# Kernel optimization log

Hardware: AMD Instinct MI355X
Metric: run time of the kernel (lower is better)

The kernel has to match this reference:

```python
import jax, jax.numpy as jnp
import numpy as np

N_NODES = 50000
N_EDGES = 600000
IC, H, OC = 64, 128, 32
EPS = 1e-5


def setup_inputs() -> dict:
    key = jax.random.key(0)
    ks = jax.random.split(key, 8)
    x = jax.random.normal(ks[0], (N_NODES, IC), dtype=jnp.float32)
    ei = jax.random.randint(ks[1], (2, N_EDGES), 0, N_NODES, dtype=jnp.int64)
    proj_w = jax.random.normal(ks[2], (IC, H), dtype=jnp.float32) * 0.05
    proj_b = jnp.zeros((H,), dtype=jnp.float32)
    # conv_w[layer, lin, :, :] with lin order: key, query, value, skip
    conv_w = jax.random.normal(ks[3], (3, 4, H, H), dtype=jnp.float32) * 0.05
    conv_b = jnp.zeros((3, 4, H), dtype=jnp.float32)
    bn_gamma = jnp.ones((3, H), dtype=jnp.float32)
    bn_beta = jnp.zeros((3, H), dtype=jnp.float32)
    head_w = jax.random.normal(ks[4], (H, OC), dtype=jnp.float32) * 0.05
    head_b = jnp.zeros((OC,), dtype=jnp.float32)
    return {"x": x, "ei": ei, "proj_w": proj_w, "proj_b": proj_b,
            "conv_w": conv_w, "conv_b": conv_b, "bn_gamma": bn_gamma,
            "bn_beta": bn_beta, "head_w": head_w, "head_b": head_b}


def _res_gated_conv(x, src, dst, w, b):
    # PyG ResGatedGraphConv: out_i = skip(x_i) + sum_j sigmoid(key(x_i)+query(x_j)) * value(x_j)
    k = x @ w[0] + b[0]      # key   (applied to target/dst)
    q = x @ w[1] + b[1]      # query (applied to source/src)
    v = x @ w[2] + b[2]      # value (applied to source/src)
    msg = jax.nn.sigmoid(k[dst] + q[src]) * v[src]          # [E, H]
    agg = jax.ops.segment_sum(msg, dst, num_segments=x.shape[0])  # [N, H]
    return x @ w[3] + b[3] + agg


def _batchnorm(x, gamma, beta):
    # training-mode BatchNorm1d: batch statistics over the node dimension
    mean = jnp.mean(x, axis=0)
    var = jnp.var(x, axis=0)
    return gamma * (x - mean) * jax.lax.rsqrt(var + EPS) + beta


def reference(x, ei, proj_w, proj_b, conv_w, conv_b, bn_gamma, bn_beta, head_w, head_b):
    src, dst = ei[0], ei[1]
    h = jax.nn.relu(x @ proj_w + proj_b)
    for layer in range(3):
        h = _res_gated_conv(h, src, dst, conv_w[layer], conv_b[layer])
        h = jax.nn.relu(_batchnorm(h, bn_gamma[layer], bn_beta[layer]))
        # dropout(p=0.2) is identity in eval mode
    return h @ head_w + head_b
```

## Files before the change

### kernel.cpp

```cpp
#include <hip/hip_runtime.h>
#include <hip/hip_bf16.h>
#include <math.h>

#define HDIM 128
#define ICDIM 64
#define OCDIM 32
#define BN_EPS 1e-5f
#define NCH 64

typedef __attribute__((ext_vector_type(8))) short bv8;
typedef __attribute__((ext_vector_type(4))) float fv4;

static __device__ __forceinline__ unsigned short f2bf(float v) {
    __hip_bfloat16 t = __float2bfloat16(v);
    return *(unsigned short*)&t;
}
static __device__ __forceinline__ float bflo(unsigned int u) {
    union { unsigned int i; float f; } c; c.i = u << 16; return c.f;
}
static __device__ __forceinline__ float bfhi(unsigned int u) {
    union { unsigned int i; float f; } c; c.i = u & 0xffff0000u; return c.f;
}
static __device__ __forceinline__ unsigned int pack2bf(float a, float b) {
    return (unsigned int)f2bf(a) | ((unsigned int)f2bf(b) << 16);
}

__global__ void wprep_kernel(const float* __restrict__ conv_w,
                             const float* __restrict__ proj_w,
                             __hip_bfloat16* __restrict__ Wt,
                             __hip_bfloat16* __restrict__ Wp) {
    int mat = blockIdx.x;
    if (mat < 12) {
        const float* s = conv_w + (size_t)mat * HDIM * HDIM;
        __hip_bfloat16* d = Wt + (size_t)mat * HDIM * HDIM;
        for (int idx = threadIdx.x; idx < HDIM * HDIM; idx += 256) {
            int i = idx >> 7, o = idx & 127;
            d[(size_t)o * HDIM + i] = __float2bfloat16(s[idx]);
        }
    } else {
        for (int idx = threadIdx.x; idx < ICDIM * HDIM; idx += 256) {
            int i = idx >> 7, o = idx & 127;
            Wp[(size_t)o * ICDIM + i] = __float2bfloat16(proj_w[idx]);
        }
    }
}

__global__ __launch_bounds__(256)
void proj_mfma_kernel(const float* __restrict__ x,
                      const __hip_bfloat16* __restrict__ wp,
                      const float* __restrict__ b,
                      __hip_bfloat16* __restrict__ h, int n) {
    __shared__ unsigned int xs[NCH * ICDIM / 2];
    int tid = threadIdx.x;
    int m0 = blockIdx.x * NCH;

    const float2* xsrc = (const float2*)(x + (size_t)m0 * ICDIM);
    for (int i = tid; i < NCH * ICDIM / 2; i += 256) {
        int node = m0 + (i >> 5);
        float2 v = (node < n) ? xsrc[i] : (float2){0.f, 0.f};
        xs[i ^ (((i >> 5) & 7) << 2)] = pack2bf(v.x, v.y);
    }

    int wv = tid >> 6;
    int lane = tid & 63;
    int j = lane & 15;
    int kg = lane >> 4;
    int sw = (j & 7) << 4;

    bv8 af[2][2];
#pragma unroll
    for (int gs = 0; gs < 2; ++gs)
#pragma unroll
        for (int ks = 0; ks < 2; ++ks)
            af[gs][ks] = *(const bv8*)((const unsigned short*)wp +
                (size_t)(wv * 32 + gs * 16 + j) * ICDIM + ks * 32 + kg * 8);

    float4 bias0 = *(const float4*)(b + wv * 32 + kg * 4);
    float4 bias1 = *(const float4*)(b + wv * 32 + 16 + kg * 4);

    __syncthreads();

#pragma unroll
    for (int t4 = 0; t4 < NCH / 16; ++t4) {
        const char* rowbase = (const char*)xs + (t4 * 16 + j) * (ICDIM * 2);
        fv4 acc0 = (fv4){0.f, 0.f, 0.f, 0.f};
        fv4 acc1 = (fv4){0.f, 0.f, 0.f, 0.f};
#pragma unroll
        for (int ks = 0; ks < 2; ++ks) {
            bv8 bf = *(const bv8*)(rowbase + ((kg * 16 + ks * 64) ^ sw));
            acc0 = __builtin_amdgcn_mfma_f32_16x16x32_bf16(af[0][ks], bf, acc0, 0, 0, 0);
            acc1 = __builtin_amdgcn_mfma_f32_16x16x32_bf16(af[1][ks], bf, acc1, 0, 0, 0);
        }
        int node = m0 + t4 * 16 + j;
        if (node < n) {
            unsigned short* o =
                (unsigned short*)h + (size_t)node * HDIM + wv * 32 + kg * 4;
            ushort4 r0, r1;
            r0.x = f2bf(fmaxf(acc0.x + bias0.x, 0.f));
            r0.y = f2bf(fmaxf(acc0.y + bias0.y, 0.f));
            r0.z = f2bf(fmaxf(acc0.z + bias0.z, 0.f));
            r0.w = f2bf(fmaxf(acc0.w + bias0.w, 0.f));
            r1.x = f2bf(fmaxf(acc1.x + bias1.x, 0.f));
            r1.y = f2bf(fmaxf(acc1.y + bias1.y, 0.f));
            r1.z = f2bf(fmaxf(acc1.z + bias1.z, 0.f));
            r1.w = f2bf(fmaxf(acc1.w + bias1.w, 0.f));
            *(ushort4*)o = r0;
            *(ushort4*)(o + 16) = r1;
        }
    }
}

__global__ __launch_bounds__(1024)
void gemm4_fused_kernel(const __hip_bfloat16* __restrict__ hB,
                        const float* __restrict__ Ssrc,
                        const float* __restrict__ stp,
                        const float* __restrict__ gma,
                        const float* __restrict__ bta,
                        const __hip_bfloat16* __restrict__ wt4,
                        const float* __restrict__ b4,
                        __hip_bfloat16* __restrict__ K,
                        unsigned int* __restrict__ QV,
                        float* __restrict__ S, int n) {
    __shared__ unsigned short hs[NCH * HDIM];
    int tid = threadIdx.x;
    int m0 = blockIdx.x * NCH;
    int wsw = ((tid >> 4) & 7) << 4;

    if (Ssrc) {
        const float4* src = (const float4*)(Ssrc + (size_t)m0 * HDIM);
        float4 v0 = src[tid * 2];
        float4 v1 = src[tid * 2 + 1];
        int c0 = (tid * 8) & 127;
        float invn = 1.f / (float)n;
        float vv[8] = {v0.x, v0.y, v0.z, v0.w, v1.x, v1.y, v1.z, v1.w};
        unsigned int* dst = (unsigned int*)((char*)hs + ((tid * 16) ^ wsw));
#pragma unroll
        for (int p = 0; p < 8; p += 2) {
            int c = c0 + p;
            float mA = stp[c] * invn, mB = stp[c + 1] * invn;
            float scA = gma[c] * rsqrtf(stp[128 + c] * invn - mA * mA + BN_EPS);
            float scB = gma[c + 1] * rsqrtf(stp[129 + c] * invn - mB * mB + BN_EPS);
            float shA = bta[c] - mA * scA, shB = bta[c + 1] - mB * scB;
            float rA = fmaxf(fmaf(vv[p], scA, shA), 0.f);
            float rB = fmaxf(fmaf(vv[p + 1], scB, shB), 0.f);
            dst[p >> 1] = pack2bf(rA, rB);
        }
    } else {
        const uint4* src = (const uint4*)((const unsigned short*)hB + (size_t)m0 * HDIM);
        *(uint4*)((char*)hs + ((tid * 16) ^ wsw)) = src[tid];
    }

    int wv = tid >> 6;
    int lane = tid & 63;
    int lin = wv >> 2;
    int g2 = wv & 3;
    int j = lane & 15;
    int kg = lane >> 4;
    int sw = (j & 7) << 4;

    const unsigned short* wbase =
        (const unsigned short*)(wt4 + (size_t)lin * HDIM * HDIM);
    bv8 af[2][4];
#pragma unroll
    for (int gs = 0; gs < 2; ++gs)
#pragma unroll
        for (int ks = 0; ks < 4; ++ks)
            af[gs][ks] = *(const bv8*)(wbase +
                (size_t)(g2 * 32 + gs * 16 + j) * HDIM + ks * 32 + kg * 8);

    const float* bl = b4 + lin * HDIM;
    float4 bias0 = *(const float4*)(bl + g2 * 32 + kg * 4);
    float4 bias1 = *(const float4*)(bl + g2 * 32 + 16 + kg * 4);

    __syncthreads();

#pragma unroll
    for (int t4 = 0; t4 < NCH / 16; ++t4) {
        const char* rowbase = (const char*)hs + (t4 * 16 + j) * (HDIM * 2);
        fv4 acc0 = (fv4){0.f, 0.f, 0.f, 0.f};
        fv4 acc1 = (fv4){0.f, 0.f, 0.f, 0.f};
#pragma unroll
        for (int ks = 0; ks < 4; ++ks) {
            bv8 bf = *(const bv8*)(rowbase + ((kg * 16 + ks * 64) ^ sw));
            acc0 = __builtin_amdgcn_mfma_f32_16x16x32_bf16(af[0][ks], bf, acc0, 0, 0, 0);
            acc1 = __builtin_amdgcn_mfma_f32_16x16x32_bf16(af[1][ks], bf, acc1, 0, 0, 0);
        }
        int node = m0 + t4 * 16 + j;
        if (node >= n) continue;
        int c0 = g2 * 32 + kg * 4;
        float f0 = acc0.x + bias0.x, f1 = acc0.y + bias0.y;
        float f2 = acc0.z + bias0.z, f3 = acc0.w + bias0.w;
        float f4 = acc1.x + bias1.x, f5 = acc1.y + bias1.y;
        float f6 = acc1.z + bias1.z, f7 = acc1.w + bias1.w;
        if (lin == 3) {
            float* o = S + (size_t)node * HDIM + c0;
            *(float4*)o = (float4){f0, f1, f2, f3};
            *(float4*)(o + 16) = (float4){f4, f5, f6, f7};
        } else if (lin == 0) {
            unsigned short* o = (unsigned short*)K + (size_t)node * HDIM + c0;
            *(ushort4*)o = (ushort4){f2bf(f0), f2bf(f1), f2bf(f2), f2bf(f3)};
            *(ushort4*)(o + 16) = (ushort4){f2bf(f4), f2bf(f5), f2bf(f6), f2bf(f7)};
        } else {
            unsigned int* o = QV + (size_t)node * HDIM + c0 + (lin - 1);
            o[0] = pack2bf(f0, f1);
            o[2] = pack2bf(f2, f3);
            o[16] = pack2bf(f4, f5);
            o[18] = pack2bf(f6, f7);
        }
    }
}

__global__ void hist_kernel(const int* __restrict__ ei, int* __restrict__ deg, int e) {
    int i = blockIdx.x * 256 + threadIdx.x;
    if (i < e) atomicAdd(&deg[ei[(size_t)e + i]], 1);
}

__global__ void scan1_kernel(const int* __restrict__ deg, int* __restrict__ incl,
                             int* __restrict__ bsum, int n) {
    __shared__ int tmp[256];
    int i = blockIdx.x * 256 + threadIdx.x;
    int v = (i < n) ? deg[i] : 0;
    tmp[threadIdx.x] = v;
    __syncthreads();
    for (int ofs = 1; ofs < 256; ofs <<= 1) {
        int t = (threadIdx.x >= ofs) ? tmp[threadIdx.x - ofs] : 0;
        __syncthreads();
        tmp[threadIdx.x] += t;
        __syncthreads();
    }
    if (i < n) incl[i] = tmp[threadIdx.x];
    if (threadIdx.x == 255) bsum[blockIdx.x] = tmp[255];
}

__global__ void scan2_kernel(int* __restrict__ bsum, int nb) {
    __shared__ int tmp[256];
    int v = (threadIdx.x < nb) ? bsum[threadIdx.x] : 0;
    tmp[threadIdx.x] = v;
    __syncthreads();
    for (int ofs = 1; ofs < 256; ofs <<= 1) {
        int t = (threadIdx.x >= ofs) ? tmp[threadIdx.x - ofs] : 0;
        __syncthreads();
        tmp[threadIdx.x] += t;
        __syncthreads();
    }
    if (threadIdx.x < nb) bsum[threadIdx.x] = tmp[threadIdx.x] - v;
}

__global__ void scan3_kernel(const int* __restrict__ deg, const int* __restrict__ incl,
                             const int* __restrict__ bsum, int* __restrict__ off,
                             int* __restrict__ cursor, int n, int e) {
    int i = blockIdx.x * 256 + threadIdx.x;
    if (i < n) {
        int ex = incl[i] - deg[i] + bsum[blockIdx.x];
        off[i] = ex;
        cursor[i] = ex;
        if (i == n - 1) off[n] = e;
    }
}

__global__ void scatter_kernel(const int* __restrict__ ei, int* __restrict__ cursor,
                               int* __restrict__ esrc, int e) {
    int i = blockIdx.x * 256 + threadIdx.x;
    if (i < e) {
        int dst = ei[(size_t)e + i];
        int pos = atomicAdd(&cursor[dst], 1);
        esrc[pos] = ei[i];
    }
}

__global__ void agg_kernel(const int* __restrict__ off, const int* __restrict__ esrc,
                           const __hip_bfloat16* __restrict__ kb,
                           const unsigned int* __restrict__ QV,
                           float* __restrict__ S, int n) {
    int d = blockIdx.x * 4 + (threadIdx.x >> 6);
    if (d >= n) return;
    int lane = threadIdx.x & 63;
    const uint2* qvw = (const uint2*)QV;
    unsigned int kwu = ((const unsigned int*)kb)[(size_t)d * 64 + lane];
    float k0 = bflo(kwu), k1 = bfhi(kwu);
    float a0 = 0.f, a1 = 0.f;

#define EDGE(u)                                               \
    {                                                         \
        float g0 = k0 + bflo(u.x), g1 = k1 + bfhi(u.x);       \
        float e0 = __expf(-g0), e1 = __expf(-g1);             \
        a0 += __fdividef(bflo(u.y), 1.f + e0);                \
        a1 += __fdividef(bfhi(u.y), 1.f + e1);                \
    }

    int j0 = off[d], s1 = off[d + 1];
    int nb = (s1 - j0) >> 2;
    uint2 cu0, cu1, cu2, cu3;
    if (nb > 0) {
        int sA = esrc[j0], sB = esrc[j0 + 1], sC = esrc[j0 + 2], sD = esrc[j0 + 3];
        cu0 = qvw[(size_t)sA * 64 + lane];
        cu1 = qvw[(size_t)sB * 64 + lane];
        cu2 = qvw[(size_t)sC * 64 + lane];
        cu3 = qvw[(size_t)sD * 64 + lane];
    }
    for (int b = 1; b < nb; ++b) {
        int jn = j0 + b * 4;
        int sA = esrc[jn], sB = esrc[jn + 1], sC = esrc[jn + 2], sD = esrc[jn + 3];
        uint2 nu0 = qvw[(size_t)sA * 64 + lane];
        uint2 nu1 = qvw[(size_t)sB * 64 + lane];
        uint2 nu2 = qvw[(size_t)sC * 64 + lane];
        uint2 nu3 = qvw[(size_t)sD * 64 + lane];
        EDGE(cu0); EDGE(cu1); EDGE(cu2); EDGE(cu3);
        cu0 = nu0; cu1 = nu1; cu2 = nu2; cu3 = nu3;
    }
    if (nb > 0) { EDGE(cu0); EDGE(cu1); EDGE(cu2); EDGE(cu3); }
    for (int j = j0 + nb * 4; j < s1; ++j) {
        int s = esrc[j];
        uint2 u = qvw[(size_t)s * 64 + lane];
        EDGE(u);
    }
#undef EDGE

    float2* sp = (float2*)(S + (size_t)d * HDIM) + lane;
    float2 old = *sp;
    old.x += a0; old.y += a1;
    *sp = old;
}

__global__ void stats_kernel(const float* __restrict__ s,
                             float* __restrict__ stats, int n) {
    int c = threadIdx.x & 127, rh = threadIdx.x >> 7;
    int r0 = blockIdx.x * 128;
    int r1 = min(r0 + 128, n);
    float sum = 0.f, sq = 0.f;
    for (int r = r0 + rh; r < r1; r += 2) {
        float v = s[(size_t)r * HDIM + c];
        sum += v;
        sq = fmaf(v, v, sq);
    }
    __shared__ float ls[2][HDIM], lq[2][HDIM];
    ls[rh][c] = sum;
    lq[rh][c] = sq;
    __syncthreads();
    if (rh == 0) {
        atomicAdd(&stats[c], ls[0][c] + ls[1][c]);
        atomicAdd(&stats[HDIM + c], lq[0][c] + lq[1][c]);
    }
}

__global__ void head_bn_kernel(const float* __restrict__ S,
                               const float* __restrict__ stats,
                               const float* __restrict__ gamma,
                               const float* __restrict__ beta,
                               const float* __restrict__ w,
                               const float* __restrict__ b,
                               float* __restrict__ out, int n) {
    __shared__ float hsm[8][HDIM];
    float invn = 1.f / (float)n;
    for (int i = threadIdx.x; i < 8 * HDIM; i += 256) {
        int r = i >> 7, c = i & 127;
        int node = blockIdx.x * 8 + r;
        float v = 0.f;
        if (node < n) {
            float mean = stats[c] * invn;
            float var = stats[128 + c] * invn - mean * mean;
            float sc = gamma[c] * rsqrtf(var + BN_EPS);
            float sh = beta[c] - mean * sc;
            v = fmaxf(fmaf(S[(size_t)node * HDIM + c], sc, sh), 0.f);
        }
        hsm[r][c] = v;
    }
    __syncthreads();
    int c = threadIdx.x & 31;
    int ng = threadIdx.x >> 5;
    int node = blockIdx.x * 8 + ng;
    if (node >= n) return;
    float acc = b[c];
#pragma unroll
    for (int k = 0; k < HDIM; ++k)
        acc = fmaf(hsm[ng][k], w[k * OCDIM + c], acc);
    out[(size_t)node * OCDIM + c] = acc;
}

extern "C" void kernel_launch(void* const* d_in, const int* in_sizes, int n_in,
                              void* d_out, int out_size, void* d_ws, size_t ws_size,
                              hipStream_t stream) {
    const float* x      = (const float*)d_in[0];
    const int*   ei     = (const int*)  d_in[1];
    const float* proj_w = (const float*)d_in[2];
    const float* proj_b = (const float*)d_in[3];
    const float* conv_w = (const float*)d_in[4];
    const float* conv_b = (const float*)d_in[5];
    const float* bn_g   = (const float*)d_in[6];
    const float* bn_b   = (const float*)d_in[7];
    const float* head_w = (const float*)d_in[8];
    const float* head_b = (const float*)d_in[9];
    float* out = (float*)d_out;

    int n = in_sizes[0] / ICDIM;
    int e = in_sizes[1] / 2;

    size_t nh = (size_t)n * HDIM;
    size_t need = nh * 4 + 768 * 4 + nh * 2 + nh * 2 + nh * 4
                + (size_t)12 * HDIM * HDIM * 2 + (size_t)HDIM * ICDIM * 2
                + ((size_t)3 * n + (n + 1) + 256 + e) * 4;
    if (ws_size < need) return;

    float* S  = (float*)d_ws;
    float* st = S + nh;
    __hip_bfloat16* h = (__hip_bfloat16*)(st + 768);
    __hip_bfloat16* K = h + nh;
    unsigned int* QV = (unsigned int*)(K + nh);
    __hip_bfloat16* Wt = (__hip_bfloat16*)(QV + nh);
    __hip_bfloat16* Wp = Wt + (size_t)12 * HDIM * HDIM;

    int* deg    = (int*)(Wp + (size_t)HDIM * ICDIM);
    int* incl   = deg + n;
    int* off    = incl + n;
    int* cursor = off + n + 1;
    int* bsum   = cursor + n;
    int* esrc   = bsum + 256;

    hipMemsetAsync(st, 0, 768 * sizeof(float), stream);
    hipMemsetAsync(deg, 0, (size_t)n * sizeof(int), stream);

    int gb_e = (e + 255) / 256;
    int gb_n = (n + 255) / 256;

    wprep_kernel<<<13, 256, 0, stream>>>(conv_w, proj_w, Wt, Wp);
    proj_mfma_kernel<<<(n + NCH - 1) / NCH, 256, 0, stream>>>(x, Wp, proj_b, h, n);

    hist_kernel<<<gb_e, 256, 0, stream>>>(ei, deg, e);
    scan1_kernel<<<gb_n, 256, 0, stream>>>(deg, incl, bsum, n);
    scan2_kernel<<<1, 256, 0, stream>>>(bsum, gb_n);
    scan3_kernel<<<gb_n, 256, 0, stream>>>(deg, incl, bsum, off, cursor, n, e);
    scatter_kernel<<<gb_e, 256, 0, stream>>>(ei, cursor, esrc, e);

    int gm = (n + NCH - 1) / NCH;
    for (int l = 0; l < 3; ++l) {
        const float* Ssrc = (l == 0) ? nullptr : S;
        const float* stp  = (l == 0) ? st : st + (size_t)(l - 1) * 256;
        const float* gma  = (l == 0) ? bn_g : bn_g + (size_t)(l - 1) * HDIM;
        const float* bta  = (l == 0) ? bn_b : bn_b + (size_t)(l - 1) * HDIM;
        gemm4_fused_kernel<<<gm, 1024, 0, stream>>>(
            h, Ssrc, stp, gma, bta,
            Wt + (size_t)l * 4 * HDIM * HDIM, conv_b + (size_t)l * 4 * HDIM,
            K, QV, S, n);
        agg_kernel<<<(n + 3) / 4, 256, 0, stream>>>(off, esrc, K, QV, S, n);
        stats_kernel<<<(n + 127) / 128, 256, 0, stream>>>(S, st + l * 256, n);
    }

    head_bn_kernel<<<(n + 7) / 8, 256, 0, stream>>>(
        S, st + 2 * 256, bn_g + 2 * HDIM, bn_b + 2 * HDIM, head_w, head_b, out, n);
}
```

Baseline: 495.9 us.

## Interleave Q/V in 4-channel groups and split edges across half-waves in aggregation

```diff
diff --git a/kernel.cpp b/kernel.cpp
--- a/kernel.cpp
+++ b/kernel.cpp
@@ -201,11 +201,10 @@
             *(ushort4*)o = (ushort4){f2bf(f0), f2bf(f1), f2bf(f2), f2bf(f3)};
             *(ushort4*)(o + 16) = (ushort4){f2bf(f4), f2bf(f5), f2bf(f6), f2bf(f7)};
         } else {
-            unsigned int* o = QV + (size_t)node * HDIM + c0 + (lin - 1);
-            o[0] = pack2bf(f0, f1);
-            o[2] = pack2bf(f2, f3);
-            o[16] = pack2bf(f4, f5);
-            o[18] = pack2bf(f6, f7);
+            unsigned short* o = (unsigned short*)QV + (size_t)node * 256 + 2 * c0
+                              + ((lin == 2) ? 4 : 0);
+            *(ushort4*)o = (ushort4){f2bf(f0), f2bf(f1), f2bf(f2), f2bf(f3)};
+            *(ushort4*)(o + 32) = (ushort4){f2bf(f4), f2bf(f5), f2bf(f6), f2bf(f7)};
         }
     }
 }
@@ -232,26 +231,23 @@
     if (threadIdx.x == 255) bsum[blockIdx.x] = tmp[255];
 }
 
-__global__ void scan2_kernel(int* __restrict__ bsum, int nb) {
+__global__ void scan23_kernel(const int* __restrict__ deg, const int* __restrict__ incl,
+                              const int* __restrict__ bsum, int* __restrict__ off,
+                              int* __restrict__ cursor, int n, int e, int nb) {
     __shared__ int tmp[256];
-    int v = (threadIdx.x < nb) ? bsum[threadIdx.x] : 0;
-    tmp[threadIdx.x] = v;
+    int t = threadIdx.x;
+    tmp[t] = (t < nb) ? bsum[t] : 0;
     __syncthreads();
     for (int ofs = 1; ofs < 256; ofs <<= 1) {
-        int t = (threadIdx.x >= ofs) ? tmp[threadIdx.x - ofs] : 0;
+        int a = (t >= ofs) ? tmp[t - ofs] : 0;
         __syncthreads();
-        tmp[threadIdx.x] += t;
+        tmp[t] += a;
         __syncthreads();
     }
-    if (threadIdx.x < nb) bsum[threadIdx.x] = tmp[threadIdx.x] - v;
-}
-
-__global__ void scan3_kernel(const int* __restrict__ deg, const int* __restrict__ incl,
-                             const int* __restrict__ bsum, int* __restrict__ off,
-                             int* __restrict__ cursor, int n, int e) {
-    int i = blockIdx.x * 256 + threadIdx.x;
+    int pre = (blockIdx.x == 0) ? 0 : tmp[blockIdx.x - 1];
+    int i = blockIdx.x * 256 + t;
     if (i < n) {
-        int ex = incl[i] - deg[i] + bsum[blockIdx.x];
+        int ex = incl[i] - deg[i] + pre;
         off[i] = ex;
         cursor[i] = ex;
         if (i == n - 1) off[n] = e;
@@ -275,51 +271,49 @@
     int d = blockIdx.x * 4 + (threadIdx.x >> 6);
     if (d >= n) return;
     int lane = threadIdx.x & 63;
-    const uint2* qvw = (const uint2*)QV;
-    unsigned int kwu = ((const unsigned int*)kb)[(size_t)d * 64 + lane];
-    float k0 = bflo(kwu), k1 = bfhi(kwu);
-    float a0 = 0.f, a1 = 0.f;
-
-#define EDGE(u)                                               \
-    {                                                         \
-        float g0 = k0 + bflo(u.x), g1 = k1 + bfhi(u.x);       \
-        float e0 = __expf(-g0), e1 = __expf(-g1);             \
-        a0 += __fdividef(bflo(u.y), 1.f + e0);                \
-        a1 += __fdividef(bfhi(u.y), 1.f + e1);                \
-    }
-
-    int j0 = off[d], s1 = off[d + 1];
-    int nb = (s1 - j0) >> 2;
-    uint2 cu0, cu1, cu2, cu3;
-    if (nb > 0) {
-        int sA = esrc[j0], sB = esrc[j0 + 1], sC = esrc[j0 + 2], sD = esrc[j0 + 3];
-        cu0 = qvw[(size_t)sA * 64 + lane];
-        cu1 = qvw[(size_t)sB * 64 + lane];
-        cu2 = qvw[(size_t)sC * 64 + lane];
-        cu3 = qvw[(size_t)sD * 64 + lane];
-    }
-    for (int b = 1; b < nb; ++b) {
-        int jn = j0 + b * 4;
-        int sA = esrc[jn], sB = esrc[jn + 1], sC = esrc[jn + 2], sD = esrc[jn + 3];
-        uint2 nu0 = qvw[(size_t)sA * 64 + lane];
-        uint2 nu1 = qvw[(size_t)sB * 64 + lane];
-        uint2 nu2 = qvw[(size_t)sC * 64 + lane];
-        uint2 nu3 = qvw[(size_t)sD * 64 + lane];
-        EDGE(cu0); EDGE(cu1); EDGE(cu2); EDGE(cu3);
-        cu0 = nu0; cu1 = nu1; cu2 = nu2; cu3 = nu3;
-    }
-    if (nb > 0) { EDGE(cu0); EDGE(cu1); EDGE(cu2); EDGE(cu3); }
-    for (int j = j0 + nb * 4; j < s1; ++j) {
-        int s = esrc[j];
-        uint2 u = qvw[(size_t)s * 64 + lane];
-        EDGE(u);
-    }
-#undef EDGE
-
-    float2* sp = (float2*)(S + (size_t)d * HDIM) + lane;
-    float2 old = *sp;
-    old.x += a0; old.y += a1;
-    *sp = old;
+    int half = lane >> 5;
+    int cl = lane & 31;
+    const char* qvb = (const char*)QV;
+
+    uint2 ku = *(const uint2*)((const unsigned short*)kb + (size_t)d * HDIM + 4 * cl);
+    float k0 = bflo(ku.x), k1 = bfhi(ku.x), k2 = bflo(ku.y), k3 = bfhi(ku.y);
+    float a0 = 0.f, a1 = 0.f, a2 = 0.f, a3 = 0.f;
+
+#define EDGE4(u)                                                     \
+    {                                                                \
+        float g0 = k0 + bflo(u.x), g1 = k1 + bfhi(u.x);              \
+        float g2 = k2 + bflo(u.y), g3 = k3 + bfhi(u.y);              \
+        a0 += __fdividef(bflo(u.z), 1.f + __expf(-g0));              \
+        a1 += __fdividef(bfhi(u.z), 1.f + __expf(-g1));              \
+        a2 += __fdividef(bflo(u.w), 1.f + __expf(-g2));              \
+        a3 += __fdividef(bfhi(u.w), 1.f + __expf(-g3));              \
+    }
+
+    int j = off[d] + half, s1 = off[d + 1];
+    for (; j + 2 < s1; j += 4) {
+        int sA = esrc[j], sB = esrc[j + 2];
+        uint4 uA = *(const uint4*)(qvb + (size_t)sA * 512 + cl * 16);
+        uint4 uB = *(const uint4*)(qvb + (size_t)sB * 512 + cl * 16);
+        EDGE4(uA);
+        EDGE4(uB);
+    }
+    if (j < s1) {
+        int sA = esrc[j];
+        uint4 uA = *(const uint4*)(qvb + (size_t)sA * 512 + cl * 16);
+        EDGE4(uA);
+    }
+#undef EDGE4
+
+    a0 += __shfl_xor(a0, 32);
+    a1 += __shfl_xor(a1, 32);
+    a2 += __shfl_xor(a2, 32);
+    a3 += __shfl_xor(a3, 32);
+    if (half == 0) {
+        float4* sp = (float4*)(S + (size_t)d * HDIM) + cl;
+        float4 o = *sp;
+        o.x += a0; o.y += a1; o.z += a2; o.w += a3;
+        *sp = o;
+    }
 }
 
 __global__ void stats_kernel(const float* __restrict__ s,
@@ -427,8 +421,7 @@
 
     hist_kernel<<<gb_e, 256, 0, stream>>>(ei, deg, e);
     scan1_kernel<<<gb_n, 256, 0, stream>>>(deg, incl, bsum, n);
-    scan2_kernel<<<1, 256, 0, stream>>>(bsum, gb_n);
-    scan3_kernel<<<gb_n, 256, 0, stream>>>(deg, incl, bsum, off, cursor, n, e);
+    scan23_kernel<<<gb_n, 256, 0, stream>>>(deg, incl, bsum, off, cursor, n, e, gb_n);
     scatter_kernel<<<gb_e, 256, 0, stream>>>(ei, cursor, esrc, e);
 
     int gm = (n + NCH - 1) / NCH;
```

Result: faster. 467.8 us (-5.7%).
